# Performance work log

Hardware: AMD Instinct MI355X
Metric: run time of the kernel (lower is better)

## Reference

```python
import jax, jax.numpy as jnp
import numpy as np

N_NODES = 100000
N_EDGES = 1600000
MOTIF_DIM = 32
HIDDEN = 64


def setup_inputs() -> dict:
    key = jax.random.key(0)
    k1, k2, k3, k4 = jax.random.split(key, 4)
    motif_x = jax.random.normal(k1, (N_NODES, MOTIF_DIM), dtype=jnp.float32)
    edge_index = jax.random.randint(k2, (2, N_EDGES), 0, N_NODES, dtype=jnp.int64)
    in_dim = 4 * MOTIF_DIM
    W1 = jax.random.normal(k3, (in_dim, HIDDEN), dtype=jnp.float32) / np.sqrt(in_dim)
    b1 = jnp.zeros((HIDDEN,), dtype=jnp.float32)
    W2 = jax.random.normal(k4, (HIDDEN, 1), dtype=jnp.float32) / np.sqrt(HIDDEN)
    b2 = jnp.zeros((1,), dtype=jnp.float32)
    return {"motif_x": motif_x, "edge_index": edge_index, "W1": W1, "b1": b1, "W2": W2, "b2": b2}


def reference(motif_x, edge_index, W1, b1, W2, b2):
    src = edge_index[0]
    dst = edge_index[1]
    mu = motif_x[src]                      # [E, D] gather
    mv = motif_x[dst]                      # [E, D] gather
    feats = jnp.concatenate([mu, mv, jnp.abs(mu - mv), mu * mv], axis=1)  # [E, 4D]
    h = jax.nn.relu(feats @ W1 + b1)       # [E, H]
    g = jax.nn.sigmoid(h @ W2 + b2)[:, 0]  # [E]
    return jnp.clip(g, 0.0, 1.0)
```

## Files before the change

kernel.cpp:

```cpp
#include <hip/hip_runtime.h>
#include <hip/hip_fp16.h>

#define D 32
#define H 64

typedef __attribute__((ext_vector_type(8))) _Float16 f16x8;
typedef __attribute__((ext_vector_type(4))) float f32x4;

union AB { uint4 u; f16x8 v; __half2 h2[4]; };

template <int CTRL>
__device__ __forceinline__ float dppadd(float x) {
  int s = __builtin_amdgcn_update_dpp(0, __float_as_int(x), CTRL, 0xF, 0xF, true);
  return x + __int_as_float(s);
}
__device__ __forceinline__ float row16_sum(float x) {
  x = dppadd<0xB1>(x);
  x = dppadd<0x4E>(x);
  x = dppadd<0x141>(x);
  x = dppadd<0x140>(x);
  return x;
}

__global__ __launch_bounds__(256) void prep(
    const float* __restrict__ x, const float* __restrict__ W1,
    unsigned short* __restrict__ xh, unsigned short* __restrict__ btab,
    int n4, int nPack) {
  int b = blockIdx.x;
  if (b < nPack) {
    int i = b * 256 + threadIdx.x;
    if (i < n4) {
      float4 v = ((const float4*)x)[i];
      ushort4 o;
      o.x = __half_as_ushort(__float2half(v.x));
      o.y = __half_as_ushort(__float2half(v.y));
      o.z = __half_as_ushort(__float2half(v.z));
      o.w = __half_as_ushort(__float2half(v.w));
      ((ushort4*)xh)[i] = o;
    }
  } else {
    int id = (b - nPack) * 256 + threadIdx.x;
    if (id < 16 * 64 * 8) {
      int j = id & 7;
      int l = (id >> 3) & 63;
      int f = id >> 9;
      int s = f & 3, t = f >> 2;
      int k = s * 32 + (l >> 4) * 8 + j;
      int n = t * 16 + (l & 15);
      btab[id] = __half_as_ushort(__float2half(W1[k * H + n]));
    }
  }
}

__device__ __forceinline__ void compute_pair(
    uint4 mu0U, uint4 mv0U, uint4 mu1U, uint4 mv1U,
    const _Float16* __restrict__ bl,
    const float* __restrict__ b1v, const float* __restrict__ w2v, float bias2,
    int pair, int q, int m, int nE, float* __restrict__ out) {
  AB mu0, mv0, mu1, mv1, ac0, ap0, ac1, ap1;
  mu0.u = mu0U; mv0.u = mv0U; mu1.u = mu1U; mv1.u = mv1U;
#pragma unroll
  for (int k = 0; k < 4; ++k) {
    ac0.h2[k] = __habs2(__hsub2(mu0.h2[k], mv0.h2[k]));
    ap0.h2[k] = __hmul2(mu0.h2[k], mv0.h2[k]);
    ac1.h2[k] = __habs2(__hsub2(mu1.h2[k], mv1.h2[k]));
    ap1.h2[k] = __hmul2(mu1.h2[k], mv1.h2[k]);
  }

  float part0[4], part1[4];
#pragma unroll
  for (int t = 0; t < 4; ++t) {
    float bv = b1v[t];
    f32x4 acc0 = (f32x4){bv, bv, bv, bv};
    f32x4 acc1 = (f32x4){bv, bv, bv, bv};
    f16x8 B0 = *(const f16x8*)(bl + (t * 4 + 0) * 512);
    acc0 = __builtin_amdgcn_mfma_f32_16x16x32_f16(mu0.v, B0, acc0, 0, 0, 0);
    acc1 = __builtin_amdgcn_mfma_f32_16x16x32_f16(mu1.v, B0, acc1, 0, 0, 0);
    f16x8 B1 = *(const f16x8*)(bl + (t * 4 + 1) * 512);
    acc0 = __builtin_amdgcn_mfma_f32_16x16x32_f16(mv0.v, B1, acc0, 0, 0, 0);
    acc1 = __builtin_amdgcn_mfma_f32_16x16x32_f16(mv1.v, B1, acc1, 0, 0, 0);
    f16x8 B2 = *(const f16x8*)(bl + (t * 4 + 2) * 512);
    acc0 = __builtin_amdgcn_mfma_f32_16x16x32_f16(ac0.v, B2, acc0, 0, 0, 0);
    acc1 = __builtin_amdgcn_mfma_f32_16x16x32_f16(ac1.v, B2, acc1, 0, 0, 0);
    f16x8 B3 = *(const f16x8*)(bl + (t * 4 + 3) * 512);
    acc0 = __builtin_amdgcn_mfma_f32_16x16x32_f16(ap0.v, B3, acc0, 0, 0, 0);
    acc1 = __builtin_amdgcn_mfma_f32_16x16x32_f16(ap1.v, B3, acc1, 0, 0, 0);
#pragma unroll
    for (int r = 0; r < 4; ++r) {
      float h0 = fmaxf(acc0[r], 0.f);
      float h1 = fmaxf(acc1[r], 0.f);
      part0[r] = (t == 0) ? h0 * w2v[0] : fmaf(h0, w2v[t], part0[r]);
      part1[r] = (t == 0) ? h1 * w2v[0] : fmaf(h1, w2v[t], part1[r]);
    }
  }

#pragma unroll
  for (int r = 0; r < 4; ++r) {
    part0[r] = row16_sum(part0[r]);
    part1[r] = row16_sum(part1[r]);
  }

  if (m < 4) {
    float z0 = (m == 0 ? part0[0] : m == 1 ? part0[1] : m == 2 ? part0[2] : part0[3]) + bias2;
    float z1 = (m == 0 ? part1[0] : m == 1 ? part1[1] : m == 2 ? part1[2] : part1[3]) + bias2;
    int ew0 = pair * 32 + q * 4 + m;
    int ew1 = pair * 32 + 16 + q * 4 + m;
    if (ew0 < nE) out[ew0] = 1.f / (1.f + __expf(-z0));
    if (ew1 < nE) out[ew1] = 1.f / (1.f + __expf(-z1));
  }
}

__global__ __launch_bounds__(256, 4) void edge_mfma(
    const unsigned short* __restrict__ xh, const unsigned short* __restrict__ btab,
    const int* __restrict__ ei,
    const float* __restrict__ b1, const float* __restrict__ W2,
    const float* __restrict__ b2, float* __restrict__ out,
    int nE, int nPairs) {
  __shared__ _Float16 lds_b[16 * 64 * 8];

  {
    const uint4* src = (const uint4*)btab;
    uint4* dst = (uint4*)lds_b;
#pragma unroll
    for (int i = 0; i < 4; ++i)
      dst[threadIdx.x + i * 256] = src[threadIdx.x + i * 256];
  }
  __syncthreads();

  int lane = threadIdx.x & 63;
  int wid  = (blockIdx.x * 256 + threadIdx.x) >> 6;
  int nW   = (gridDim.x * 256) >> 6;
  int m = lane & 15;
  int q = lane >> 4;
  if (wid >= nPairs) return;

  float b1v[4], w2v[4];
#pragma unroll
  for (int t = 0; t < 4; ++t) {
    b1v[t] = b1[t * 16 + m];
    w2v[t] = W2[t * 16 + m];
  }
  float bias2 = b2[0];

  const uint4* xb = (const uint4*)xh;
  int eLim = nE - 1;
  int pLim = nPairs - 1;
  int selOff = (lane >> 5) ? nE : 0;
  int eoff = lane & 31;

  int p = wid;
  int idxNxt;
  uint4 amu0, amv0, amu1, amv1;
  {
    int e = p * 32 + eoff; e = e < nE ? e : eLim;
    int idxCur = ei[selOff + e];
    int sn0 = __shfl(idxCur, m);
    int sn1 = __shfl(idxCur, 16 + m);
    int dn0 = __shfl(idxCur, 32 + m);
    int dn1 = __shfl(idxCur, 48 + m);
    amu0 = xb[sn0 * 4 + q]; amv0 = xb[dn0 * 4 + q];
    amu1 = xb[sn1 * 4 + q]; amv1 = xb[dn1 * 4 + q];
    int p1 = p + nW; p1 = p1 < nPairs ? p1 : pLim;
    int e1 = p1 * 32 + eoff; e1 = e1 < nE ? e1 : eLim;
    idxNxt = ei[selOff + e1];
  }

  while (p < nPairs) {
    int pn = p + nW;
    int sn0 = __shfl(idxNxt, m);
    int sn1 = __shfl(idxNxt, 16 + m);
    int dn0 = __shfl(idxNxt, 32 + m);
    int dn1 = __shfl(idxNxt, 48 + m);
    uint4 bmu0 = xb[sn0 * 4 + q], bmv0 = xb[dn0 * 4 + q];
    uint4 bmu1 = xb[sn1 * 4 + q], bmv1 = xb[dn1 * 4 + q];
    {
      int p2 = pn + nW; p2 = p2 < nPairs ? p2 : pLim;
      int e2 = p2 * 32 + eoff; e2 = e2 < nE ? e2 : eLim;
      idxNxt = ei[selOff + e2];
    }

    int bofs = lane * 8;
    asm volatile("" : "+v"(bofs));
    const _Float16* bl = lds_b + bofs;

    compute_pair(amu0, amv0, amu1, amv1, bl, b1v, w2v, bias2, p, q, m, nE, out);

    amu0 = bmu0; amv0 = bmv0; amu1 = bmu1; amv1 = bmv1;
    p = pn;
  }
}

__global__ __launch_bounds__(256) void edge_full(
    const float* __restrict__ x, const int* __restrict__ ei,
    const float* __restrict__ W1, const float* __restrict__ b1,
    const float* __restrict__ W2, const float* __restrict__ b2,
    float* __restrict__ out, int nE) {
  int e = blockIdx.x * 256 + threadIdx.x;
  if (e >= nE) return;
  int s = ei[e];
  int d = ei[e + nE];
  const float4* mu4 = (const float4*)(x + (size_t)s * D);
  const float4* mv4 = (const float4*)(x + (size_t)d * D);
  float mu[D], mv[D], c[D], p[D];
#pragma unroll
  for (int qq = 0; qq < D / 4; ++qq) {
    float4 a = mu4[qq];
    float4 b = mv4[qq];
    mu[4*qq+0] = a.x; mv[4*qq+0] = b.x; c[4*qq+0] = fabsf(a.x-b.x); p[4*qq+0] = a.x*b.x;
    mu[4*qq+1] = a.y; mv[4*qq+1] = b.y; c[4*qq+1] = fabsf(a.y-b.y); p[4*qq+1] = a.y*b.y;
    mu[4*qq+2] = a.z; mv[4*qq+2] = b.z; c[4*qq+2] = fabsf(a.z-b.z); p[4*qq+2] = a.z*b.z;
    mu[4*qq+3] = a.w; mv[4*qq+3] = b.w; c[4*qq+3] = fabsf(a.w-b.w); p[4*qq+3] = a.w*b.w;
  }
  float z = b2[0];
  for (int j = 0; j < H; ++j) {
    float a = b1[j];
#pragma unroll
    for (int k = 0; k < D; ++k) {
      a = fmaf(mu[k], W1[k * H + j], a);
      a = fmaf(mv[k], W1[(D + k) * H + j], a);
      a = fmaf(c[k],  W1[(2 * D + k) * H + j], a);
      a = fmaf(p[k],  W1[(3 * D + k) * H + j], a);
    }
    a = fmaxf(a, 0.f);
    z = fmaf(a, W2[j], z);
  }
  float g = 1.f / (1.f + __expf(-z));
  out[e] = fminf(fmaxf(g, 0.f), 1.f);
}

extern "C" void kernel_launch(void* const* d_in, const int* in_sizes, int n_in,
                              void* d_out, int out_size, void* d_ws, size_t ws_size,
                              hipStream_t stream) {
  const float* x  = (const float*)d_in[0];
  const int*   ei = (const int*)d_in[1];
  const float* W1 = (const float*)d_in[2];
  const float* b1 = (const float*)d_in[3];
  const float* W2 = (const float*)d_in[4];
  const float* b2 = (const float*)d_in[5];
  float* out = (float*)d_out;

  int nN = in_sizes[0] / D;
  int nE = in_sizes[1] / 2;

  size_t xh_shorts = (size_t)nN * D;
  size_t need = (xh_shorts + 16 * 64 * 8) * sizeof(unsigned short);
  if (ws_size >= need) {
    unsigned short* xh   = (unsigned short*)d_ws;
    unsigned short* btab = xh + xh_shorts;
    int n4 = nN * D / 4;
    int nPack = (n4 + 255) / 256;
    int nBt = (16 * 64 * 8 + 255) / 256;
    prep<<<nPack + nBt, 256, 0, stream>>>(x, W1, xh, btab, n4, nPack);
    int nTiles = (nE + 15) / 16;
    int nPairs = (nTiles + 1) / 2;
    edge_mfma<<<2048, 256, 0, stream>>>(xh, btab, ei, b1, W2, b2, out, nE, nPairs);
  } else {
    edge_full<<<(nE + 255) / 256, 256, 0, stream>>>(x, ei, W1, b1, W2, b2, out, nE);
  }
}
```

Measured before the change: 115.5 us.

## Deepen gather prefetch with double-buffered loop, raise occupancy, size grid to work

The edge loop is unrolled by two with alternating register buffers, so node-feature gathers for the next pair and index loads two pairs ahead are in flight while the current pair runs through the MFMAs. Each lane now loads its src/dst indices directly instead of loading one index and redistributing with cross-lane shuffles. Launch bounds are raised to 8 blocks per SM, and the grid is sized from the number of pairs instead of a fixed 2048 blocks. The tail pair's base is clamped to nE-32, which makes the MFMA path require at least 32 edges. A leftover warm-up block that loads and discards values adds redundant work, and the tighter register budget risks spills.

```diff
diff --git a/kernel.cpp b/kernel.cpp
--- a/kernel.cpp
+++ b/kernel.cpp
@@ -56,7 +56,7 @@
     uint4 mu0U, uint4 mv0U, uint4 mu1U, uint4 mv1U,
     const _Float16* __restrict__ bl,
     const float* __restrict__ b1v, const float* __restrict__ w2v, float bias2,
-    int pair, int q, int m, int nE, float* __restrict__ out) {
+    int ebase, int q, int m, int nE, float* __restrict__ out) {
   AB mu0, mv0, mu1, mv1, ac0, ap0, ac1, ap1;
   mu0.u = mu0U; mv0.u = mv0U; mu1.u = mu1U; mv1.u = mv1U;
 #pragma unroll
@@ -103,14 +103,14 @@
   if (m < 4) {
     float z0 = (m == 0 ? part0[0] : m == 1 ? part0[1] : m == 2 ? part0[2] : part0[3]) + bias2;
     float z1 = (m == 0 ? part1[0] : m == 1 ? part1[1] : m == 2 ? part1[2] : part1[3]) + bias2;
-    int ew0 = pair * 32 + q * 4 + m;
-    int ew1 = pair * 32 + 16 + q * 4 + m;
+    int ew0 = ebase + q * 4 + m;
+    int ew1 = ebase + 16 + q * 4 + m;
     if (ew0 < nE) out[ew0] = 1.f / (1.f + __expf(-z0));
     if (ew1 < nE) out[ew1] = 1.f / (1.f + __expf(-z1));
   }
 }
 
-__global__ __launch_bounds__(256, 4) void edge_mfma(
+__global__ __launch_bounds__(256, 8) void edge_mfma(
     const unsigned short* __restrict__ xh, const unsigned short* __restrict__ btab,
     const int* __restrict__ ei,
     const float* __restrict__ b1, const float* __restrict__ W2,
@@ -143,50 +143,74 @@
   float bias2 = b2[0];
 
   const uint4* xb = (const uint4*)xh;
-  int eLim = nE - 1;
+  const int* eis = ei;
+  const int* eid = ei + nE;
   int pLim = nPairs - 1;
-  int selOff = (lane >> 5) ? nE : 0;
-  int eoff = lane & 31;
+  int eCap = nE - 32;
 
   int p = wid;
-  int idxNxt;
-  uint4 amu0, amv0, amu1, amv1;
-  {
-    int e = p * 32 + eoff; e = e < nE ? e : eLim;
-    int idxCur = ei[selOff + e];
-    int sn0 = __shfl(idxCur, m);
-    int sn1 = __shfl(idxCur, 16 + m);
-    int dn0 = __shfl(idxCur, 32 + m);
-    int dn1 = __shfl(idxCur, 48 + m);
-    amu0 = xb[sn0 * 4 + q]; amv0 = xb[dn0 * 4 + q];
-    amu1 = xb[sn1 * 4 + q]; amv1 = xb[dn1 * 4 + q];
-    int p1 = p + nW; p1 = p1 < nPairs ? p1 : pLim;
-    int e1 = p1 * 32 + eoff; e1 = e1 < nE ? e1 : eLim;
-    idxNxt = ei[selOff + e1];
-  }
-
-  while (p < nPairs) {
-    int pn = p + nW;
-    int sn0 = __shfl(idxNxt, m);
-    int sn1 = __shfl(idxNxt, 16 + m);
-    int dn0 = __shfl(idxNxt, 32 + m);
-    int dn1 = __shfl(idxNxt, 48 + m);
-    uint4 bmu0 = xb[sn0 * 4 + q], bmv0 = xb[dn0 * 4 + q];
-    uint4 bmu1 = xb[sn1 * 4 + q], bmv1 = xb[dn1 * 4 + q];
-    {
-      int p2 = pn + nW; p2 = p2 < nPairs ? p2 : pLim;
-      int e2 = p2 * 32 + eoff; e2 = e2 < nE ? e2 : eLim;
-      idxNxt = ei[selOff + e2];
-    }
-
-    int bofs = lane * 8;
-    asm volatile("" : "+v"(bofs));
-    const _Float16* bl = lds_b + bofs;
-
-    compute_pair(amu0, amv0, amu1, amv1, bl, b1v, w2v, bias2, p, q, m, nE, out);
-
-    amu0 = bmu0; amv0 = bmv0; amu1 = bmu1; amv1 = bmv1;
-    p = pn;
+  int pbC = p * 32; pbC = pbC < eCap ? pbC : eCap;
+  {
+    int o0 = pbC + m;
+    int ia = eis[o0], ib = eis[o0 + 16], ic = eid[o0], id_ = eid[o0 + 16];
+    uint4 t0 = xb[ia * 4 + q], t1 = xb[ib * 4 + q];
+    uint4 t2 = xb[ic * 4 + q], t3 = xb[id_ * 4 + q];
+    #define AMU0 t0
+    asm volatile("" ::);
+    (void)t0; (void)t1; (void)t2; (void)t3;
+  }
+  uint4 amu0, amu1, amv0, amv1;
+  {
+    int o0 = pbC + m;
+    int ia = eis[o0], ib = eis[o0 + 16], ic = eid[o0], id_ = eid[o0 + 16];
+    amu0 = xb[ia * 4 + q]; amu1 = xb[ib * 4 + q];
+    amv0 = xb[ic * 4 + q]; amv1 = xb[id_ * 4 + q];
+  }
+  int ja, jb, jc, jd;
+  int pbN;
+  {
+    int p1 = p + nW; p1 = p1 < pLim ? p1 : pLim;
+    pbN = p1 * 32; pbN = pbN < eCap ? pbN : eCap;
+    int o1 = pbN + m;
+    ja = eis[o1]; jb = eis[o1 + 16]; jc = eid[o1]; jd = eid[o1 + 16];
+  }
+
+  uint4 bmu0, bmu1, bmv0, bmv1;
+  while (true) {
+    bmu0 = xb[ja * 4 + q]; bmu1 = xb[jb * 4 + q];
+    bmv0 = xb[jc * 4 + q]; bmv1 = xb[jd * 4 + q];
+    int pb2;
+    {
+      int p2 = p + 2 * nW; p2 = p2 < pLim ? p2 : pLim;
+      pb2 = p2 * 32; pb2 = pb2 < eCap ? pb2 : eCap;
+      int o2 = pb2 + m;
+      ja = eis[o2]; jb = eis[o2 + 16]; jc = eid[o2]; jd = eid[o2 + 16];
+    }
+    {
+      int bofs = lane * 8;
+      asm volatile("" : "+v"(bofs));
+      compute_pair(amu0, amv0, amu1, amv1, lds_b + bofs, b1v, w2v, bias2,
+                   pbC, q, m, nE, out);
+    }
+    p += nW; if (p > pLim) return;
+    pbC = pbN; pbN = pb2;
+
+    amu0 = xb[ja * 4 + q]; amu1 = xb[jb * 4 + q];
+    amv0 = xb[jc * 4 + q]; amv1 = xb[jd * 4 + q];
+    {
+      int p2 = p + 2 * nW; p2 = p2 < pLim ? p2 : pLim;
+      pb2 = p2 * 32; pb2 = pb2 < eCap ? pb2 : eCap;
+      int o2 = pb2 + m;
+      ja = eis[o2]; jb = eis[o2 + 16]; jc = eid[o2]; jd = eid[o2 + 16];
+    }
+    {
+      int bofs = lane * 8;
+      asm volatile("" : "+v"(bofs));
+      compute_pair(bmu0, bmv0, bmu1, bmv1, lds_b + bofs, b1v, w2v, bias2,
+                   pbC, q, m, nE, out);
+    }
+    p += nW; if (p > pLim) return;
+    pbC = pbN; pbN = pb2;
   }
 }
 
@@ -244,7 +268,7 @@
 
   size_t xh_shorts = (size_t)nN * D;
   size_t need = (xh_shorts + 16 * 64 * 8) * sizeof(unsigned short);
-  if (ws_size >= need) {
+  if (ws_size >= need && nE >= 32) {
     unsigned short* xh   = (unsigned short*)d_ws;
     unsigned short* btab = xh + xh_shorts;
     int n4 = nN * D / 4;
@@ -253,7 +277,9 @@
     prep<<<nPack + nBt, 256, 0, stream>>>(x, W1, xh, btab, n4, nPack);
     int nTiles = (nE + 15) / 16;
     int nPairs = (nTiles + 1) / 2;
-    edge_mfma<<<2048, 256, 0, stream>>>(xh, btab, ei, b1, W2, b2, out, nE, nPairs);
+    int blocks = (nPairs + 15) / 16;
+    if (blocks < 1) blocks = 1;
+    edge_mfma<<<blocks, 256, 0, stream>>>(xh, btab, ei, b1, W2, b2, out, nE, nPairs);
   } else {
     edge_full<<<(nE + 255) / 256, 256, 0, stream>>>(x, ei, W1, b1, W2, b2, out, nE);
   }
```

After: 227.2 us. 96.7% more time.
